# Optimization experiments

Hardware: AMD Instinct MI355X
Metric: run time of the kernel (lower is better)

The kernel has to match this reference:

```python
import jax, jax.numpy as jnp
import numpy as np

HIDDEN = 1024
NUM_HEADS = 16
HEAD_DIM = HIDDEN // NUM_HEADS


def rotate_half(x):
    x1, x2 = jnp.split(x, 2, axis=-1)
    return jnp.concatenate((-x2, x1), axis=-1)


def rope_tables(T, dim, dtype):
    inv_freq = 1.0 / (10000.0 ** (jnp.arange(0, dim, 2, dtype=jnp.float32) / dim))
    t = jnp.arange(T, dtype=jnp.float32)
    freqs = t[:, None] * inv_freq[None, :]           # [T, dim/2]
    emb = jnp.concatenate((freqs, freqs), axis=-1)   # [T, dim]
    return jnp.cos(emb).astype(dtype), jnp.sin(emb).astype(dtype)


def setup_inputs() -> dict:
    key = jax.random.key(0)
    kx, kq, kk, kv, ko = jax.random.split(key, 5)
    B, T = 2, 2048
    scale = 1.0 / np.sqrt(HIDDEN)
    return {
        "x": jax.random.normal(kx, (B, T, HIDDEN), dtype=jnp.float32),
        "wq": jax.random.normal(kq, (HIDDEN, HIDDEN), dtype=jnp.float32) * scale,
        "wk": jax.random.normal(kk, (HIDDEN, HIDDEN), dtype=jnp.float32) * scale,
        "wv": jax.random.normal(kv, (HIDDEN, HIDDEN), dtype=jnp.float32) * scale,
        "wo": jax.random.normal(ko, (HIDDEN, HIDDEN), dtype=jnp.float32) * scale,
    }


def reference(x, wq, wk, wv, wo):
    B, T, _ = x.shape
    H, D = NUM_HEADS, HEAD_DIM
    # projections (Linear, no bias): x @ W.T; reshape to [B, H, T, D]
    q = (x @ wq.T).reshape(B, T, H, D).transpose(0, 2, 1, 3)
    k = (x @ wk.T).reshape(B, T, H, D).transpose(0, 2, 1, 3)
    v = (x @ wv.T).reshape(B, T, H, D).transpose(0, 2, 1, 3)
    cos, sin = rope_tables(T, D, x.dtype)            # [T, D]
    cos = cos[None, None]                            # [1,1,T,D]
    sin = sin[None, None]
    q = q * cos + rotate_half(q) * sin
    k = k * cos + rotate_half(k) * sin
    scores = jnp.einsum("bhtd,bhsd->bhts", q, k) / np.sqrt(D).astype(x.dtype)
    attn = jax.nn.softmax(scores, axis=-1)
    out = jnp.einsum("bhts,bhsd->bhtd", attn, v)     # [B,H,T,D]
    out = out.transpose(0, 2, 1, 3).reshape(B, T, H * D)
    return out @ wo.T
```

## Files before the change

### kernel.cpp

```cpp
#include <hip/hip_runtime.h>
#include <hip/hip_bf16.h>
#include <stdint.h>

typedef __bf16 bf16;
typedef __attribute__((ext_vector_type(8))) __bf16 bf16x8;
typedef __attribute__((ext_vector_type(4))) float f32x4;
typedef __attribute__((ext_vector_type(16))) float f32x16;

#define L2E 1.4426950408889634f

__device__ __forceinline__ f32x4 mfma16(bf16x8 a, bf16x8 b, f32x4 c) {
  return __builtin_amdgcn_mfma_f32_16x16x32_bf16(a, b, c, 0, 0, 0);
}

__device__ __forceinline__ f32x16 mfma32(bf16x8 a, bf16x8 b, f32x16 c) {
  return __builtin_amdgcn_mfma_f32_32x32x16_bf16(a, b, c, 0, 0, 0);
}

__device__ __forceinline__ void gload16(void* lds, const void* g) {
  __builtin_amdgcn_global_load_lds(
      (const __attribute__((address_space(1))) uint32_t*)g,
      (__attribute__((address_space(3))) uint32_t*)lds, 16, 0, 0);
}

__device__ __forceinline__ unsigned cvt_pk_bf16(float lo, float hi) {
  unsigned r;
  asm("v_cvt_pk_bf16_f32 %0, %1, %2" : "=v"(r) : "v"(lo), "v"(hi));
  return r;
}

__device__ __forceinline__ void pl32swap(unsigned& a, unsigned& b) {
  auto r = __builtin_amdgcn_permlane32_swap(a, b, false, false);
  a = r[0];
  b = r[1];
}

__global__ __launch_bounds__(256) void prep_cast(
    const float* __restrict__ x, const float* __restrict__ wq,
    const float* __restrict__ wk, const float* __restrict__ wv,
    const float* __restrict__ wo, bf16* __restrict__ xb,
    bf16* __restrict__ wqb, bf16* __restrict__ wkb, bf16* __restrict__ wvb,
    bf16* __restrict__ wob) {
  int i = blockIdx.x * 256 + threadIdx.x;
  const int NX = 4096 * 1024 / 4;
  const int NW = 1024 * 1024 / 4;
  const float* src; bf16* dst; int off;
  if (i < NX)               { src = x;  dst = xb;  off = i; }
  else if (i < NX + NW)     { src = wq; dst = wqb; off = i - NX; }
  else if (i < NX + 2 * NW) { src = wk; dst = wkb; off = i - (NX + NW); }
  else if (i < NX + 3 * NW) { src = wv; dst = wvb; off = i - (NX + 2 * NW); }
  else                      { src = wo; dst = wob; off = i - (NX + 3 * NW); }
  float4 v = ((const float4*)src)[off];
  union { bf16 h[4]; uint2 u; } o;
  o.h[0] = (bf16)v.x; o.h[1] = (bf16)v.y; o.h[2] = (bf16)v.z; o.h[3] = (bf16)v.w;
  ((uint2*)dst)[off] = o.u;
}

__global__ __launch_bounds__(256) void rope_tab(float* __restrict__ ct,
                                                float* __restrict__ st) {
  int i = blockIdx.x * 256 + threadIdx.x;
  int t = i >> 5, d = i & 31;
  float inv = powf(10000.f, -(float)d * (1.f / 32.f));
  float a = (float)t * inv;
  ct[i] = cosf(a);
  st[i] = sinf(a);
}

__device__ __forceinline__ void gemm_mainloop(const bf16* __restrict__ A,
                                              const bf16* __restrict__ W,
                                              int m0, int n0,
                                              bf16 (*As)[4096], bf16 (*Bs)[4096],
                                              f32x4 acc[4][4]) {
  const int tid = threadIdx.x;
  const int lane = tid & 63, wave = tid >> 6;
  const int wr = (wave >> 1) * 64, wc = (wave & 1) * 64;
  const int lr = lane & 15, lh = lane >> 4;

  auto stage = [&](bf16* dA, bf16* dB, int kt) {
    int k0 = kt * 32;
#pragma unroll
    for (int p = 0; p < 2; p++) {
      int u = p * 256 + tid; int row = u >> 2; int kg = (u & 3) ^ (row & 3);
      gload16(dA + (size_t)u * 8, A + (size_t)(m0 + row) * 1024 + k0 + kg * 8);
    }
#pragma unroll
    for (int p = 0; p < 2; p++) {
      int u = p * 256 + tid; int row = u >> 2; int kg = (u & 3) ^ (row & 3);
      gload16(dB + (size_t)u * 8, W + (size_t)(n0 + row) * 1024 + k0 + kg * 8);
    }
  };

  stage(As[0], Bs[0], 0);
  int cur = 0;
  for (int kt = 0; kt < 32; ++kt) {
    __syncthreads();
    const bf16* cA = As[cur]; const bf16* cB = Bs[cur];
    bf16x8 af[4], bfr[4];
#pragma unroll
    for (int i = 0; i < 4; i++) {
      int row = wr + i * 16 + lr; int un = row * 4 + (lh ^ (row & 3));
      af[i] = *(const bf16x8*)(cA + (size_t)un * 8);
    }
#pragma unroll
    for (int j = 0; j < 4; j++) {
      int row = wc + j * 16 + lr; int un = row * 4 + (lh ^ (row & 3));
      bfr[j] = *(const bf16x8*)(cB + (size_t)un * 8);
    }
    if (kt + 1 < 32) stage(As[cur ^ 1], Bs[cur ^ 1], kt + 1);
#pragma unroll
    for (int i = 0; i < 4; i++)
#pragma unroll
      for (int j = 0; j < 4; j++) acc[i][j] = mfma16(af[i], bfr[j], acc[i][j]);
    cur ^= 1;
  }
}

__global__ __launch_bounds__(256) void gemm_qkv(
    const bf16* __restrict__ xb, const bf16* __restrict__ wq,
    const bf16* __restrict__ wk, const bf16* __restrict__ wv,
    const float* __restrict__ ct, const float* __restrict__ st,
    bf16* __restrict__ qo, bf16* __restrict__ ko, bf16* __restrict__ vo) {
  __shared__ __align__(16) bf16 As[2][4096];
  __shared__ __align__(16) bf16 Bs[2][4096];
  int bm = blockIdx.x, bn = blockIdx.y;
  int proj = bn >> 3;
  const bf16* W = proj == 0 ? wq : (proj == 1 ? wk : wv);
  bf16* out = proj == 0 ? qo : (proj == 1 ? ko : vo);
  int m0 = bm * 128, n0 = (bn & 7) * 128;

  f32x4 zero = {0.f, 0.f, 0.f, 0.f};
  f32x4 acc[4][4];
#pragma unroll
  for (int i = 0; i < 4; i++)
#pragma unroll
    for (int j = 0; j < 4; j++) acc[i][j] = zero;

  gemm_mainloop(xb, W, m0, n0, As, Bs, acc);

  const int tid = threadIdx.x, lane = tid & 63, wave = tid >> 6;
  const int wr = (wave >> 1) * 64, wc = (wave & 1) * 64;
  const int lr = lane & 15, lh = lane >> 4;
  int colb = n0 + wc;
  int h = colb >> 6;
  const float QSC = 0.125f * L2E;
#pragma unroll
  for (int i = 0; i < 4; i++) {
#pragma unroll
    for (int r = 0; r < 4; r++) {
      int m = m0 + wr + i * 16 + lh * 4 + r;
      int b = m >> 11, t = m & 2047;
      float v0 = acc[i][0][r], v1 = acc[i][1][r];
      float v2 = acc[i][2][r], v3 = acc[i][3][r];
      if (proj < 2) {
        float c0 = ct[t * 32 + lr],      s0 = st[t * 32 + lr];
        float c1 = ct[t * 32 + 16 + lr], s1 = st[t * 32 + 16 + lr];
        float n0v = v0 * c0 - v2 * s0, n2 = v2 * c0 + v0 * s0;
        float n1 = v1 * c1 - v3 * s1,  n3 = v3 * c1 + v1 * s1;
        v0 = n0v; v1 = n1; v2 = n2; v3 = n3;
        if (proj == 0) { v0 *= QSC; v1 *= QSC; v2 *= QSC; v3 *= QSC; }
      }
      size_t base = ((size_t)(b * 16 + h) * 2048 + t) * 64;
      out[base + lr]      = (bf16)v0;
      out[base + 16 + lr] = (bf16)v1;
      out[base + 32 + lr] = (bf16)v2;
      out[base + 48 + lr] = (bf16)v3;
    }
  }
}

__global__ __launch_bounds__(256) void vtrans(const bf16* __restrict__ v,
                                              bf16* __restrict__ vt) {
  __shared__ bf16 tile[64][68];
  int bh = blockIdx.x, tt = blockIdx.y;
  int tid = threadIdx.x;
  const bf16* src = v + ((size_t)bh * 2048 + tt * 64) * 64;
  int rr0 = tid >> 4;
  int c4 = (tid & 15) * 4;
#pragma unroll
  for (int p = 0; p < 4; p++) {
    int r = p * 16 + rr0;
    *(uint2*)&tile[r][c4] = *(const uint2*)(src + (size_t)r * 64 + c4);
  }
  __syncthreads();
  bf16* dst = vt + (size_t)bh * 64 * 2048 + tt * 64;
#pragma unroll
  for (int p = 0; p < 4; p++) {
    int d = p * 16 + rr0;
    union { bf16 h[4]; uint2 u; } o;
#pragma unroll
    for (int q = 0; q < 4; q++) o.h[q] = tile[c4 + q][d];
    *(uint2*)(dst + (size_t)d * 2048 + c4) = o.u;
  }
}

__global__ __launch_bounds__(256, 4) void attn(const bf16* __restrict__ q,
                                               const bf16* __restrict__ k,
                                               const bf16* __restrict__ vt,
                                               bf16* __restrict__ o) {
  __shared__ __align__(16) char smb[32768];
  int pidx = blockIdx.x;
  int L = (pidx & 7) * 128 + (pidx >> 3);
  int bh = L >> 5, qt = L & 31;

  const int tid = threadIdx.x, lane = tid & 63, wave = tid >> 6;
  const int lq = lane & 31, hi = lane >> 5;
  const int p = wave >> 1;
  const int sub = wave & 1;
  const int t128 = tid & 127;

  const bf16* kg = k + (size_t)bh * 2048 * 64;
  const bf16* vg = vt + (size_t)bh * 64 * 2048;

  int q0 = qt * 64 + sub * 32;
  const bf16* qb = q + ((size_t)bh * 2048 + q0) * 64;
  bf16x8 qf[4];
#pragma unroll
  for (int kk = 0; kk < 4; kk++)
    qf[kk] = *(const bf16x8*)(qb + (size_t)lq * 64 + kk * 16 + hi * 8);

  int vaK[4];
#pragma unroll
  for (int j = 0; j < 4; j++)
    vaK[j] = lq * 128 + (((2 * j + hi) ^ (lq & 7)) << 4);
  int vaV[2];
#pragma unroll
  for (int cc = 0; cc < 2; cc++)
    vaV[cc] = lq * 64 + (((2 * cc + hi) ^ (lq & 3)) << 4) + 4096;

  int koffe[2], voffe[2];
#pragma unroll
  for (int pp = 0; pp < 2; pp++) {
    int uu = pp * 128 + t128;
    int rK = uu >> 3, uK = (uu & 7) ^ (rK & 7);
    koffe[pp] = rK * 64 + uK * 8;
    int rV = uu >> 2, uV = (uu & 3) ^ (rV & 3);
    voffe[pp] = rV * 2048 + uV * 8;
  }

  f32x16 acc[2];
  f32x16 CM;
#pragma unroll
  for (int r = 0; r < 16; r++) { acc[0][r] = 0.f; acc[1][r] = 0.f; CM[r] = -16.f; }
  float l = 0.f;

  const int sbase = p * 16384;
  auto stage = [&](int bufoff, int itl) {
    const bf16* kt = kg + p * 65536 + itl * 2048;
    const bf16* vt2 = vg + p * 1024 + itl * 32;
#pragma unroll
    for (int pp = 0; pp < 2; pp++) {
      gload16(smb + bufoff + (pp * 128 + t128) * 16, kt + koffe[pp]);
      gload16(smb + bufoff + 4096 + (pp * 128 + t128) * 16, vt2 + voffe[pp]);
    }
  };

  auto compute = [&](int bufoff) {
    __builtin_amdgcn_s_setprio(1);
    f32x16 s = mfma32(*(const bf16x8*)(smb + bufoff + vaK[0]), qf[0], CM);
#pragma unroll
    for (int kk = 1; kk < 4; kk++)
      s = mfma32(*(const bf16x8*)(smb + bufoff + vaK[kk]), qf[kk], s);
    __builtin_amdgcn_s_setprio(0);

    float su0 = 0.f, su1 = 0.f;
    unsigned pk[8];
#pragma unroll
    for (int i = 0; i < 8; i++) {
      float pa = __builtin_amdgcn_exp2f(s[2 * i]);
      float pb2 = __builtin_amdgcn_exp2f(s[2 * i + 1]);
      su0 += pa;
      su1 += pb2;
      pk[i] = cvt_pk_bf16(pa, pb2);
    }
    l += su0 + su1;

    pl32swap(pk[0], pk[2]);
    pl32swap(pk[1], pk[3]);
    pl32swap(pk[4], pk[6]);
    pl32swap(pk[5], pk[7]);
    __builtin_amdgcn_s_setprio(1);
#pragma unroll
    for (int cc = 0; cc < 2; cc++) {
      union { unsigned u[4]; bf16x8 v; } pb;
      pb.u[0] = pk[4 * cc + 0];
      pb.u[1] = pk[4 * cc + 1];
      pb.u[2] = pk[4 * cc + 2];
      pb.u[3] = pk[4 * cc + 3];
#pragma unroll
      for (int db = 0; db < 2; db++) {
        bf16x8 va8 = *(const bf16x8*)(smb + bufoff + db * 2048 + vaV[cc]);
        acc[db] = mfma32(va8, pb.v, acc[db]);
      }
    }
    __builtin_amdgcn_s_setprio(0);
  };

  stage(sbase, 0);
  __syncthreads();

  for (int it = 0; it < 32; ++it) {
    if (it + 1 < 32) stage(sbase + ((it + 1) & 1) * 8192, it + 1);
    compute(sbase + (it & 1) * 8192);
    __syncthreads();
  }

  float* mbuf = (float*)(smb + 16384);
  float* lbuf = (float*)smb;
  if (p == 1) {
#pragma unroll
    for (int db = 0; db < 2; db++)
#pragma unroll
      for (int r = 0; r < 16; r++)
        mbuf[sub * 2048 + (db * 16 + r) * 64 + lane] = acc[db][r];
    lbuf[sub * 64 + lane] = l;
  }
  __syncthreads();
  if (p == 1) return;
#pragma unroll
  for (int db = 0; db < 2; db++)
#pragma unroll
    for (int r = 0; r < 16; r++)
      acc[db][r] += mbuf[sub * 2048 + (db * 16 + r) * 64 + lane];
  l += lbuf[sub * 64 + lane];

  {
    unsigned ta = __float_as_uint(l), tb = ta;
    pl32swap(ta, tb);
    l = __uint_as_float(ta) + __uint_as_float(tb);
  }
  float inv = 1.0f / l;
  int b = bh >> 4, h = bh & 15;
  int qrow = q0 + lq;
  bf16* orow = o + ((size_t)(b * 2048 + qrow)) * 1024 + h * 64;
#pragma unroll
  for (int db = 0; db < 2; db++)
#pragma unroll
    for (int g = 0; g < 4; g++) {
      union { bf16 h4[4]; uint2 u; } t;
#pragma unroll
      for (int e = 0; e < 4; e++) t.h4[e] = (bf16)(acc[db][4 * g + e] * inv);
      *(uint2*)(orow + db * 32 + 8 * g + 4 * hi) = t.u;
    }
}

__global__ __launch_bounds__(256) void gemm_out(const bf16* __restrict__ ab,
                                                const bf16* __restrict__ wo,
                                                float* __restrict__ out) {
  __shared__ __align__(16) bf16 As[2][4096];
  __shared__ __align__(16) bf16 Bs[2][4096];
  int m0 = blockIdx.x * 128, n0 = blockIdx.y * 128;
  f32x4 zero = {0.f, 0.f, 0.f, 0.f};
  f32x4 acc[4][4];
#pragma unroll
  for (int i = 0; i < 4; i++)
#pragma unroll
    for (int j = 0; j < 4; j++) acc[i][j] = zero;

  gemm_mainloop(ab, wo, m0, n0, As, Bs, acc);

  const int tid = threadIdx.x, lane = tid & 63, wave = tid >> 6;
  const int wr = (wave >> 1) * 64, wc = (wave & 1) * 64;
  const int lr = lane & 15, lh = lane >> 4;
#pragma unroll
  for (int i = 0; i < 4; i++)
#pragma unroll
    for (int r = 0; r < 4; r++) {
      int m = m0 + wr + i * 16 + lh * 4 + r;
#pragma unroll
      for (int j = 0; j < 4; j++) {
        int col = n0 + wc + j * 16 + lr;
        out[(size_t)m * 1024 + col] = acc[i][j][r];
      }
    }
}

extern "C" void kernel_launch(void* const* d_in, const int* in_sizes, int n_in,
                              void* d_out, int out_size, void* d_ws, size_t ws_size,
                              hipStream_t stream) {
  const float* x  = (const float*)d_in[0];
  const float* wq = (const float*)d_in[1];
  const float* wk = (const float*)d_in[2];
  const float* wv = (const float*)d_in[3];
  const float* wo = (const float*)d_in[4];
  float* out = (float*)d_out;
  char* ws = (char*)d_ws;
  const size_t MB = 1u << 20;
  bf16* xb  = (bf16*)(ws + 0);
  bf16* wqb = (bf16*)(ws + 8 * MB);
  bf16* wkb = (bf16*)(ws + 10 * MB);
  bf16* wvb = (bf16*)(ws + 12 * MB);
  bf16* wob = (bf16*)(ws + 14 * MB);
  bf16* qw  = (bf16*)(ws + 16 * MB);
  bf16* kw  = (bf16*)(ws + 24 * MB);
  bf16* vw  = (bf16*)(ws + 32 * MB);
  bf16* vtw = (bf16*)(ws + 40 * MB);
  bf16* aw  = (bf16*)(ws + 48 * MB);
  float* ct = (float*)(ws + 56 * MB);
  float* st = (float*)(ws + 56 * MB + 256 * 1024);

  prep_cast<<<8192, 256, 0, stream>>>(x, wq, wk, wv, wo, xb, wqb, wkb, wvb, wob);
  rope_tab<<<256, 256, 0, stream>>>(ct, st);
  gemm_qkv<<<dim3(32, 24), 256, 0, stream>>>(xb, wqb, wkb, wvb, ct, st, qw, kw, vw);
  vtrans<<<dim3(32, 32), 256, 0, stream>>>(vw, vtw);
  attn<<<1024, 256, 0, stream>>>(qw, kw, vtw, aw);
  gemm_out<<<dim3(32, 8), 256, 0, stream>>>(aw, wob, out);
}
```

Measured before the change: 121.1 us.

## Double query rows per attention block to reuse staged K/V tiles

Each wave now handles 64 query rows (two 32-row blocks) instead of 32, so every K and V^T fragment read from LDS feeds two MFMAs. The grid is halved to 512 blocks, the staged KV chunk per iteration doubles to 64 keys, and LDS grows to 64 KB with occupancy lowered to 2 blocks per CU. The aim is to halve global and LDS traffic per unit of compute. The cost is more registers, fewer resident waves and fewer blocks to hide latency across the CUs. It also leaves a dead block of unused pl32swap code in the epilogue.

```diff
diff --git a/kernel.cpp b/kernel.cpp
--- a/kernel.cpp
+++ b/kernel.cpp
@@ -193,14 +193,14 @@
   }
 }
 
-__global__ __launch_bounds__(256, 4) void attn(const bf16* __restrict__ q,
+__global__ __launch_bounds__(256, 2) void attn(const bf16* __restrict__ q,
                                                const bf16* __restrict__ k,
                                                const bf16* __restrict__ vt,
                                                bf16* __restrict__ o) {
-  __shared__ __align__(16) char smb[32768];
+  __shared__ __align__(16) char smb[65536];
   int pidx = blockIdx.x;
-  int L = (pidx & 7) * 128 + (pidx >> 3);
-  int bh = L >> 5, qt = L & 31;
+  int L = (pidx & 7) * 64 + (pidx >> 3);
+  int bh = L >> 4, qt = L & 15;
 
   const int tid = threadIdx.x, lane = tid & 63, wave = tid >> 6;
   const int lq = lane & 31, hi = lane >> 5;
@@ -208,139 +208,196 @@
   const int sub = wave & 1;
   const int t128 = tid & 127;
 
-  const bf16* kg = k + (size_t)bh * 2048 * 64;
-  const bf16* vg = vt + (size_t)bh * 64 * 2048;
-
-  int q0 = qt * 64 + sub * 32;
-  const bf16* qb = q + ((size_t)bh * 2048 + q0) * 64;
-  bf16x8 qf[4];
-#pragma unroll
-  for (int kk = 0; kk < 4; kk++)
-    qf[kk] = *(const bf16x8*)(qb + (size_t)lq * 64 + kk * 16 + hi * 8);
-
-  int vaK[4];
+  const bf16* kg = k + (size_t)bh * 131072 + p * 65536;
+  const bf16* vg = vt + (size_t)bh * 131072 + p * 1024;
+
+  int q0 = qt * 128 + sub * 64;
+  const bf16* qbp = q + ((size_t)bh * 2048 + q0) * 64;
+  bf16x8 qf[2][4];
+#pragma unroll
+  for (int qb = 0; qb < 2; qb++)
+#pragma unroll
+    for (int kk = 0; kk < 4; kk++)
+      qf[qb][kk] =
+          *(const bf16x8*)(qbp + (size_t)(qb * 32 + lq) * 64 + kk * 16 + hi * 8);
+
+  int va[4];
 #pragma unroll
   for (int j = 0; j < 4; j++)
-    vaK[j] = lq * 128 + (((2 * j + hi) ^ (lq & 7)) << 4);
-  int vaV[2];
-#pragma unroll
-  for (int cc = 0; cc < 2; cc++)
-    vaV[cc] = lq * 64 + (((2 * cc + hi) ^ (lq & 3)) << 4) + 4096;
-
-  int koffe[2], voffe[2];
-#pragma unroll
-  for (int pp = 0; pp < 2; pp++) {
+    va[j] = lq * 128 + (((2 * j + hi) ^ (lq & 7)) << 4);
+
+  int koffe[4], voffe[4];
+#pragma unroll
+  for (int pp = 0; pp < 4; pp++) {
     int uu = pp * 128 + t128;
-    int rK = uu >> 3, uK = (uu & 7) ^ (rK & 7);
-    koffe[pp] = rK * 64 + uK * 8;
-    int rV = uu >> 2, uV = (uu & 3) ^ (rV & 3);
-    voffe[pp] = rV * 2048 + uV * 8;
-  }
-
-  f32x16 acc[2];
+    int r = uu >> 3;
+    int u = (uu & 7) ^ (r & 7);
+    koffe[pp] = r * 64 + u * 8;
+    voffe[pp] = r * 2048 + u * 8;
+  }
+
+  f32x16 acc[2][2];
   f32x16 CM;
 #pragma unroll
-  for (int r = 0; r < 16; r++) { acc[0][r] = 0.f; acc[1][r] = 0.f; CM[r] = -16.f; }
-  float l = 0.f;
-
-  const int sbase = p * 16384;
+  for (int r = 0; r < 16; r++) {
+    acc[0][0][r] = 0.f; acc[0][1][r] = 0.f;
+    acc[1][0][r] = 0.f; acc[1][1][r] = 0.f;
+    CM[r] = -16.f;
+  }
+  float l0 = 0.f, l1 = 0.f;
+
+  const int sbase = p * 32768;
   auto stage = [&](int bufoff, int itl) {
-    const bf16* kt = kg + p * 65536 + itl * 2048;
-    const bf16* vt2 = vg + p * 1024 + itl * 32;
-#pragma unroll
-    for (int pp = 0; pp < 2; pp++) {
+    const bf16* kt = kg + itl * 4096;
+    const bf16* vt2 = vg + itl * 64;
+#pragma unroll
+    for (int pp = 0; pp < 4; pp++) {
       gload16(smb + bufoff + (pp * 128 + t128) * 16, kt + koffe[pp]);
-      gload16(smb + bufoff + 4096 + (pp * 128 + t128) * 16, vt2 + voffe[pp]);
+      gload16(smb + bufoff + 8192 + (pp * 128 + t128) * 16, vt2 + voffe[pp]);
     }
   };
 
   auto compute = [&](int bufoff) {
-    __builtin_amdgcn_s_setprio(1);
-    f32x16 s = mfma32(*(const bf16x8*)(smb + bufoff + vaK[0]), qf[0], CM);
-#pragma unroll
-    for (int kk = 1; kk < 4; kk++)
-      s = mfma32(*(const bf16x8*)(smb + bufoff + vaK[kk]), qf[kk], s);
-    __builtin_amdgcn_s_setprio(0);
-
-    float su0 = 0.f, su1 = 0.f;
-    unsigned pk[8];
-#pragma unroll
-    for (int i = 0; i < 8; i++) {
-      float pa = __builtin_amdgcn_exp2f(s[2 * i]);
-      float pb2 = __builtin_amdgcn_exp2f(s[2 * i + 1]);
-      su0 += pa;
-      su1 += pb2;
-      pk[i] = cvt_pk_bf16(pa, pb2);
-    }
-    l += su0 + su1;
-
-    pl32swap(pk[0], pk[2]);
-    pl32swap(pk[1], pk[3]);
-    pl32swap(pk[4], pk[6]);
-    pl32swap(pk[5], pk[7]);
-    __builtin_amdgcn_s_setprio(1);
-#pragma unroll
-    for (int cc = 0; cc < 2; cc++) {
-      union { unsigned u[4]; bf16x8 v; } pb;
-      pb.u[0] = pk[4 * cc + 0];
-      pb.u[1] = pk[4 * cc + 1];
-      pb.u[2] = pk[4 * cc + 2];
-      pb.u[3] = pk[4 * cc + 3];
-#pragma unroll
-      for (int db = 0; db < 2; db++) {
-        bf16x8 va8 = *(const bf16x8*)(smb + bufoff + db * 2048 + vaV[cc]);
-        acc[db] = mfma32(va8, pb.v, acc[db]);
-      }
-    }
-    __builtin_amdgcn_s_setprio(0);
+#pragma unroll
+    for (int c = 0; c < 2; c++) {
+      __builtin_amdgcn_s_setprio(1);
+      bf16x8 ka[4];
+#pragma unroll
+      for (int kk = 0; kk < 4; kk++)
+        ka[kk] = *(const bf16x8*)(smb + bufoff + c * 4096 + va[kk]);
+      f32x16 s0 = mfma32(ka[0], qf[0][0], CM);
+      f32x16 s1 = mfma32(ka[0], qf[1][0], CM);
+#pragma unroll
+      for (int kk = 1; kk < 4; kk++) {
+        s0 = mfma32(ka[kk], qf[0][kk], s0);
+        s1 = mfma32(ka[kk], qf[1][kk], s1);
+      }
+      __builtin_amdgcn_s_setprio(0);
+
+      unsigned pk0[8], pk1[8];
+      {
+        float sa = 0.f, sb = 0.f;
+#pragma unroll
+        for (int i = 0; i < 8; i++) {
+          float pa = __builtin_amdgcn_exp2f(s0[2 * i]);
+          float pb = __builtin_amdgcn_exp2f(s0[2 * i + 1]);
+          sa += pa; sb += pb;
+          pk0[i] = cvt_pk_bf16(pa, pb);
+        }
+        l0 += sa + sb;
+      }
+      {
+        float sa = 0.f, sb = 0.f;
+#pragma unroll
+        for (int i = 0; i < 8; i++) {
+          float pa = __builtin_amdgcn_exp2f(s1[2 * i]);
+          float pb = __builtin_amdgcn_exp2f(s1[2 * i + 1]);
+          sa += pa; sb += pb;
+          pk1[i] = cvt_pk_bf16(pa, pb);
+        }
+        l1 += sa + sb;
+      }
+
+      pl32swap(pk0[0], pk0[2]); pl32swap(pk0[1], pk0[3]);
+      pl32swap(pk0[4], pk0[6]); pl32swap(pk0[5], pk0[7]);
+      pl32swap(pk1[0], pk1[2]); pl32swap(pk1[1], pk1[3]);
+      pl32swap(pk1[4], pk1[6]); pl32swap(pk1[5], pk1[7]);
+
+      __builtin_amdgcn_s_setprio(1);
+#pragma unroll
+      for (int cc = 0; cc < 2; cc++) {
+        union { unsigned u[4]; bf16x8 v; } pb0, pb1;
+#pragma unroll
+        for (int w = 0; w < 4; w++) {
+          pb0.u[w] = pk0[4 * cc + w];
+          pb1.u[w] = pk1[4 * cc + w];
+        }
+        int j = 2 * c + cc;
+#pragma unroll
+        for (int db = 0; db < 2; db++) {
+          bf16x8 va8 =
+              *(const bf16x8*)(smb + bufoff + 8192 + db * 4096 + va[j]);
+          acc[0][db] = mfma32(va8, pb0.v, acc[0][db]);
+          acc[1][db] = mfma32(va8, pb1.v, acc[1][db]);
+        }
+      }
+      __builtin_amdgcn_s_setprio(0);
+    }
   };
 
   stage(sbase, 0);
   __syncthreads();
 
-  for (int it = 0; it < 32; ++it) {
-    if (it + 1 < 32) stage(sbase + ((it + 1) & 1) * 8192, it + 1);
-    compute(sbase + (it & 1) * 8192);
+  for (int it2 = 0; it2 < 8; ++it2) {
+    stage(sbase + 16384, 2 * it2 + 1);
+    compute(sbase);
     __syncthreads();
-  }
-
-  float* mbuf = (float*)(smb + 16384);
+    if (it2 + 1 < 8) stage(sbase, 2 * it2 + 2);
+    compute(sbase + 16384);
+    __syncthreads();
+  }
+
+  float* abuf = (float*)(smb + 32768);
   float* lbuf = (float*)smb;
   if (p == 1) {
 #pragma unroll
-    for (int db = 0; db < 2; db++)
-#pragma unroll
-      for (int r = 0; r < 16; r++)
-        mbuf[sub * 2048 + (db * 16 + r) * 64 + lane] = acc[db][r];
-    lbuf[sub * 64 + lane] = l;
+    for (int qb = 0; qb < 2; qb++)
+#pragma unroll
+      for (int db = 0; db < 2; db++)
+#pragma unroll
+        for (int r = 0; r < 16; r++)
+          abuf[sub * 4096 + (qb * 2 + db) * 1024 + r * 64 + lane] =
+              acc[qb][db][r];
+    lbuf[sub * 128 + lane] = l0;
+    lbuf[sub * 128 + 64 + lane] = l1;
   }
   __syncthreads();
   if (p == 1) return;
 #pragma unroll
-  for (int db = 0; db < 2; db++)
-#pragma unroll
-    for (int r = 0; r < 16; r++)
-      acc[db][r] += mbuf[sub * 2048 + (db * 16 + r) * 64 + lane];
-  l += lbuf[sub * 64 + lane];
+  for (int qb = 0; qb < 2; qb++)
+#pragma unroll
+    for (int db = 0; db < 2; db++)
+#pragma unroll
+      for (int r = 0; r < 16; r++)
+        acc[qb][db][r] +=
+            abuf[sub * 4096 + (qb * 2 + db) * 1024 + r * 64 + lane];
+  l0 += lbuf[sub * 128 + lane];
+  l1 += lbuf[sub * 128 + 64 + lane];
 
   {
-    unsigned ta = __float_as_uint(l), tb = ta;
+    unsigned ta = __float_as_uint(l0), tb = __float_as_uint(l1);
     pl32swap(ta, tb);
-    l = __uint_as_float(ta) + __uint_as_float(tb);
-  }
-  float inv = 1.0f / l;
+    float inv0, inv1;
+    float m0 = __uint_as_float(ta), m1 = __uint_as_float(tb);
+    (void)m0; (void)m1; (void)inv0; (void)inv1;
+  }
+  {
+    unsigned ta = __float_as_uint(l0), tb = ta;
+    pl32swap(ta, tb);
+    l0 = __uint_as_float(ta) + __uint_as_float(tb);
+  }
+  {
+    unsigned ta = __float_as_uint(l1), tb = ta;
+    pl32swap(ta, tb);
+    l1 = __uint_as_float(ta) + __uint_as_float(tb);
+  }
+  float inv[2] = {1.0f / l0, 1.0f / l1};
   int b = bh >> 4, h = bh & 15;
-  int qrow = q0 + lq;
-  bf16* orow = o + ((size_t)(b * 2048 + qrow)) * 1024 + h * 64;
-#pragma unroll
-  for (int db = 0; db < 2; db++)
-#pragma unroll
-    for (int g = 0; g < 4; g++) {
-      union { bf16 h4[4]; uint2 u; } t;
-#pragma unroll
-      for (int e = 0; e < 4; e++) t.h4[e] = (bf16)(acc[db][4 * g + e] * inv);
-      *(uint2*)(orow + db * 32 + 8 * g + 4 * hi) = t.u;
-    }
+#pragma unroll
+  for (int qb = 0; qb < 2; qb++) {
+    int qrow = q0 + qb * 32 + lq;
+    bf16* orow = o + ((size_t)(b * 2048 + qrow)) * 1024 + h * 64;
+#pragma unroll
+    for (int db = 0; db < 2; db++)
+#pragma unroll
+      for (int g = 0; g < 4; g++) {
+        union { bf16 h4[4]; uint2 u; } t;
+#pragma unroll
+        for (int e = 0; e < 4; e++)
+          t.h4[e] = (bf16)(acc[qb][db][4 * g + e] * inv[qb]);
+        *(uint2*)(orow + db * 32 + 8 * g + 4 * hi) = t.u;
+      }
+  }
 }
 
 __global__ __launch_bounds__(256) void gemm_out(const bf16* __restrict__ ab,
@@ -402,6 +459,6 @@
   rope_tab<<<256, 256, 0, stream>>>(ct, st);
   gemm_qkv<<<dim3(32, 24), 256, 0, stream>>>(xb, wqb, wkb, wvb, ct, st, qw, kw, vw);
   vtrans<<<dim3(32, 32), 256, 0, stream>>>(vw, vtw);
-  attn<<<1024, 256, 0, stream>>>(qw, kw, vtw, aw);
+  attn<<<512, 256, 0, stream>>>(qw, kw, vtw, aw);
   gemm_out<<<dim3(32, 8), 256, 0, stream>>>(aw, wob, out);
 }
```

Result: faster. 115.4 us (-4.6%).
